# Kernel tuning notes

Hardware: AMD Instinct MI355X
Metric: run time of the kernel (lower is better)

The kernel has to match this reference:

```python
import jax, jax.numpy as jnp
import numpy as np

N_HEADS = 16
D_HEAD = 64


def setup_inputs() -> dict:
    key = jax.random.key(0)
    ks = jax.random.split(key, 9)
    B, L, D = 2, 2048, 1024
    s = 0.02  # small init scale for weights
    return {
        "x": jax.random.normal(ks[0], (B, L, D), jnp.float32),
        "Wq": jax.random.normal(ks[1], (D, D), jnp.float32) * s,
        "bq": jax.random.normal(ks[2], (D,), jnp.float32) * s,
        "Wk": jax.random.normal(ks[3], (D, D), jnp.float32) * s,
        "bk": jax.random.normal(ks[4], (D,), jnp.float32) * s,
        "Wv": jax.random.normal(ks[5], (D, D), jnp.float32) * s,
        "bv": jax.random.normal(ks[6], (D,), jnp.float32) * s,
        "Wo": jax.random.normal(ks[7], (D, D), jnp.float32) * s,
        "bo": jax.random.normal(ks[8], (D,), jnp.float32) * s,
    }


def _alibi_bias(L, n_heads, dtype):
    # slopes m_i = 1 / x**(i+1), x = (2**8)**(1/n_heads)
    x = (2.0 ** 8) ** (1.0 / n_heads)
    slopes = jnp.asarray([1.0 / x ** (i + 1) for i in range(n_heads)], dtype=dtype)
    pos = jnp.arange(L)
    rel = (pos[None, :] - pos[:, None]).astype(dtype)  # [L, L], (j - i)
    return slopes[:, None, None] * rel[None, :, :]      # [H, L, L]


def reference(x, Wq, bq, Wk, bk, Wv, bv, Wo, bo):
    B, L, D = x.shape
    H, dh = N_HEADS, D_HEAD
    scale = dh ** -0.5
    q = (x @ Wq + bq).reshape(B, L, H, dh)
    k = (x @ Wk + bk).reshape(B, L, H, dh)
    v = (x @ Wv + bv).reshape(B, L, H, dh)
    scores = jnp.einsum("blhd,bmhd->bhlm", q, k) * scale  # [B,H,L,L]
    bias = _alibi_bias(L, H, scores.dtype)                 # [H,L,L]
    attn = jax.nn.softmax(scores + bias[None], axis=-1)
    out = jnp.einsum("bhlm,bmhd->blhd", attn, v).reshape(B, L, D)
    return out @ Wo + bo
```

## Files before the change

kernel.cpp:

```cpp
#include <hip/hip_runtime.h>
#include <cstdint>
#include <cstddef>

typedef unsigned short u16;
typedef unsigned int u32;
typedef __bf16 bf16x8 __attribute__((ext_vector_type(8)));
typedef float f32x4 __attribute__((ext_vector_type(4)));
typedef u32 u32x2 __attribute__((ext_vector_type(2)));
typedef u32 u32x4 __attribute__((ext_vector_type(4)));
typedef unsigned short u16x8 __attribute__((ext_vector_type(8)));
typedef short s16x4 __attribute__((ext_vector_type(4)));

__device__ __forceinline__ u16 f2bf(float f) {
    u32 u = __float_as_uint(f);
    u += 0x7fffu + ((u >> 16) & 1u);
    return (u16)(u >> 16);
}

__device__ __forceinline__ float fexp2(float x) {
    float r;
    asm("v_exp_f32 %0, %1" : "=v"(r) : "v"(x));
    return r;
}

__device__ __forceinline__ void gl16(const void* g, void* l) {
    __builtin_amdgcn_global_load_lds(
        (const __attribute__((address_space(1))) unsigned int*)g,
        (__attribute__((address_space(3))) unsigned int*)l, 16, 0, 0);
}

__global__ __launch_bounds__(256) void cvt_all_k(const float* __restrict__ Wq,
                                                 const float* __restrict__ Wk,
                                                 const float* __restrict__ Wv,
                                                 const float* __restrict__ Wo,
                                                 const float* __restrict__ x,
                                                 u16* __restrict__ oqkv,
                                                 u16* __restrict__ oo,
                                                 u16* __restrict__ ox) {
    const int z = blockIdx.z;
    const int bx = blockIdx.x, by = blockIdx.y;
    const int t = threadIdx.x;
    if (z >= 4) {
        int i = ((z - 4) * 256 + by * 16 + bx) * 256 + t;
        const float4* xv = (const float4*)x;
        float4 a = xv[2 * i], b = xv[2 * i + 1];
        ushort4 r0, r1;
        r0.x = f2bf(a.x); r0.y = f2bf(a.y); r0.z = f2bf(a.z); r0.w = f2bf(a.w);
        r1.x = f2bf(b.x); r1.y = f2bf(b.y); r1.z = f2bf(b.z); r1.w = f2bf(b.w);
        ((ushort4*)ox)[2 * i] = r0;
        ((ushort4*)ox)[2 * i + 1] = r1;
        return;
    }
    __shared__ float tile[64][65];
    const float* W = (z == 0) ? Wq : (z == 1) ? Wk : (z == 2) ? Wv : Wo;
    u16* o = (z < 3) ? (oqkv + ((size_t)z << 20)) : oo;
    const int tn = t & 63, tr = t >> 6;
#pragma unroll
    for (int r = 0; r < 16; ++r) {
        int kk = r * 4 + tr;
        tile[kk][tn] = W[(size_t)(by * 64 + kk) * 1024 + bx * 64 + tn];
    }
    __syncthreads();
#pragma unroll
    for (int r = 0; r < 16; ++r) {
        int nn = r * 4 + tr;
        o[(size_t)(bx * 64 + nn) * 1024 + by * 64 + tn] = f2bf(tile[tn][nn]);
    }
}

template <int MODE>
__global__ __launch_bounds__(256) void gemm_k(
    const u16* __restrict__ A, const u16* __restrict__ Bt,
    const float* __restrict__ bias0, const float* __restrict__ bias1,
    const float* __restrict__ bias2,
    u16* __restrict__ oq, u16* __restrict__ ok_, u16* __restrict__ ov,
    float* __restrict__ oc) {
    __shared__ __align__(16) u16 sh[2 * 3 * 128 * 32];
    u16* As = sh;
    u16* Bs = sh + 3 * 128 * 32;
    const int t = threadIdx.x, w = t >> 6, lane = t & 63;
    const int lr = lane & 15, lg = lane >> 4;
    const int brow = blockIdx.x * 128, bcol = blockIdx.y * 128;
    const int wr = w >> 1, wc = w & 1;
    const char* Ab = (const char*)A + (size_t)brow * 2048;
    const char* Bb = (const char*)Bt + (size_t)bcol * 2048;
    const int lrow = lane >> 2;
    const int lcol = (((lane & 3) ^ ((lane >> 3) & 3)) << 4);
    const int r0a = w * 32, r0b = w * 32 + 16;
    const size_t ga = (size_t)(r0a + lrow) * 2048 + lcol;
    const size_t gb = (size_t)(r0b + lrow) * 2048 + lcol;
    const int rsw = ((lg ^ ((lr >> 1) & 3)) << 4);

    f32x4 acc[4][4];
#pragma unroll
    for (int m = 0; m < 4; ++m)
#pragma unroll
        for (int n = 0; n < 4; ++n) acc[m][n] = (f32x4){0.f, 0.f, 0.f, 0.f};

    gl16(Ab + ga, (char*)As + r0a * 64);
    gl16(Ab + gb, (char*)As + r0b * 64);
    gl16(Bb + ga, (char*)Bs + r0a * 64);
    gl16(Bb + gb, (char*)Bs + r0b * 64);
    gl16(Ab + ga + 64, (char*)As + 8192 + r0a * 64);
    gl16(Ab + gb + 64, (char*)As + 8192 + r0b * 64);
    gl16(Bb + ga + 64, (char*)Bs + 8192 + r0a * 64);
    gl16(Bb + gb + 64, (char*)Bs + 8192 + r0b * 64);

    for (int tt = 0; tt < 32; ++tt) {
        if (tt < 31) {
            asm volatile("s_waitcnt vmcnt(4)" ::: "memory");
        } else {
            asm volatile("s_waitcnt vmcnt(0)" ::: "memory");
        }
        __builtin_amdgcn_s_barrier();
        __builtin_amdgcn_sched_barrier(0);
        if (tt < 30) {
            const int nb = (tt + 2) % 3;
            const size_t ko = (size_t)(tt + 2) * 64;
            char* Asn = (char*)As + nb * 8192;
            char* Bsn = (char*)Bs + nb * 8192;
            gl16(Ab + ga + ko, Asn + r0a * 64);
            gl16(Ab + gb + ko, Asn + r0b * 64);
            gl16(Bb + ga + ko, Bsn + r0a * 64);
            gl16(Bb + gb + ko, Bsn + r0b * 64);
        }
        const char* AsB = (const char*)As + (tt % 3) * 8192;
        const char* BsB = (const char*)Bs + (tt % 3) * 8192;
        bf16x8 af[4], bfr[4];
#pragma unroll
        for (int m = 0; m < 4; ++m)
            af[m] = *(const bf16x8*)(AsB + (wr * 64 + m * 16 + lr) * 64 + rsw);
#pragma unroll
        for (int n = 0; n < 4; ++n)
            bfr[n] = *(const bf16x8*)(BsB + (wc * 64 + n * 16 + lr) * 64 + rsw);
#pragma unroll
        for (int m = 0; m < 4; ++m)
#pragma unroll
            for (int n = 0; n < 4; ++n)
                acc[m][n] = __builtin_amdgcn_mfma_f32_16x16x32_bf16(af[m], bfr[n],
                                                                    acc[m][n], 0, 0, 0);
    }

    const float QSCALE = 0.125f * 1.44269504f;
    if (MODE == 0 && bcol >= 2048) {
        const int b = brow >> 11, l0 = brow & 2047;
        __syncthreads();
#pragma unroll
        for (int n = 0; n < 4; ++n) {
            const int cl = wc * 64 + n * 16 + lr;
            const float bb2 = bias2[bcol - 2048 + cl];
#pragma unroll
            for (int m = 0; m < 4; ++m)
#pragma unroll
                for (int r = 0; r < 4; ++r) {
                    int ll = wr * 64 + m * 16 + 4 * lg + r;
                    sh[cl * 136 + ll] = f2bf(acc[m][n][r] + bb2);
                }
        }
        __syncthreads();
        const int rr = t >> 1, hf = t & 1;
        const u16* src = sh + rr * 136 + hf * 64;
        u16* dst = ov + ((size_t)b * 1024 + (bcol - 2048) + rr) * 2048 +
                   l0 + hf * 64;
#pragma unroll
        for (int i = 0; i < 8; ++i)
            *(u16x8*)(dst + i * 8) = *(const u16x8*)(src + i * 8);
        return;
    }
#pragma unroll
    for (int n = 0; n < 4; ++n) {
        const int col = bcol + wc * 64 + n * 16 + lr;
        if (MODE == 0) {
#pragma unroll
            for (int m = 0; m < 4; ++m)
#pragma unroll
                for (int r = 0; r < 4; ++r) {
                    int row = brow + wr * 64 + m * 16 + 4 * lg + r;
                    int b = row >> 11, l = row & 2047;
                    float val = acc[m][n][r];
                    if (col < 1024) {
                        int hh = col >> 6, d = col & 63;
                        oq[(((size_t)b * 16 + hh) * 2048 + l) * 64 + d] =
                            f2bf((val + bias0[col]) * QSCALE);
                    } else {
                        int c = col - 1024, hh = c >> 6, d = c & 63;
                        ok_[(((size_t)b * 16 + hh) * 2048 + l) * 64 + d] =
                            f2bf(val + bias1[c]);
                    }
                }
        } else {
            const float bb = bias0[col];
#pragma unroll
            for (int m = 0; m < 4; ++m)
#pragma unroll
                for (int r = 0; r < 4; ++r) {
                    int row = brow + wr * 64 + m * 16 + 4 * lg + r;
                    oc[(size_t)row * 1024 + col] = acc[m][n][r] + bb;
                }
        }
    }
}

__global__ __launch_bounds__(256, 2) void attn_k(const u16* __restrict__ qg_,
                                                 const u16* __restrict__ kg_,
                                                 const u16* __restrict__ vg_,
                                                 u16* __restrict__ ao) {
    __shared__ __align__(16) u16 smem[32768];
    char* Kbase = (char*)smem;
    char* Vbase = (char*)smem + 32768;
    const int t = threadIdx.x, w = t >> 6, lane = t & 63;
    const int lr = lane & 15, lg = lane >> 4;
    const int bid = blockIdx.y * 16 + blockIdx.x;
    const int qt = (bid >> 3) & 15;
    const int bh = ((bid >> 7) << 3) | (bid & 7);
    const int q0 = qt * 128, h = bh & 15, bb = bh >> 4;
    const float sl2 = exp2f(-0.5f * (float)(h + 1)) * 1.44269504f;

    const char* khead = (const char*)(kg_ + (size_t)bh * 2048 * 64);
    const char* vhead = (const char*)(vg_ + (size_t)bh * 64 * 2048);

    const int krow = lane >> 3, ku = lane & 7;
    const int kso = (w * 32 + krow) * 128 + ((ku ^ (krow & 7)) << 4);
    const int kdo = w * 4096;
    const int vrow = lane >> 4, vgr = lane & 15;
    int vso[4];
#pragma unroll
    for (int i = 0; i < 4; ++i)
        vso[i] = (w * 16 + 4 * i + vrow) * 4096 +
                 ((vgr ^ ((4 * i + vrow) & 7)) << 4);
    const int vdo = w * 4096;

    const char* qpA = (const char*)qg_ +
                      ((size_t)bh * 2048 + q0 + w * 32 + lr) * 128;
    bf16x8 qa0A = *(const bf16x8*)(qpA + lg * 16);
    bf16x8 qa1A = *(const bf16x8*)(qpA + 64 + lg * 16);
    bf16x8 qa0B = *(const bf16x8*)(qpA + 2048 + lg * 16);
    bf16x8 qa1B = *(const bf16x8*)(qpA + 2048 + 64 + lg * 16);

    f32x4 abF2[8];
#pragma unroll
    for (int n = 0; n < 8; ++n)
#pragma unroll
        for (int r = 0; r < 4; ++r)
            abF2[n][r] = sl2 * (float)(n * 16 + 4 * lg + r - 2047) - 16.0f;
    const float ainc = sl2 * 128.0f;
    f32x4 oaccA[4], oaccB[4];
#pragma unroll
    for (int nn = 0; nn < 4; ++nn) {
        oaccA[nn] = (f32x4){0.f, 0.f, 0.f, 0.f};
        oaccB[nn] = (f32x4){0.f, 0.f, 0.f, 0.f};
    }
    f32x4 laccA = (f32x4){0.f, 0.f, 0.f, 0.f};
    f32x4 laccB = (f32x4){0.f, 0.f, 0.f, 0.f};
    const u32x4 ones32 = {0x3F803F80u, 0x3F803F80u, 0x3F803F80u, 0x3F803F80u};
    const bf16x8 onesf = __builtin_bit_cast(bf16x8, ones32);

    {
        char* kd = Kbase + kdo;
        char* vd = Vbase + vdo;
#pragma unroll
        for (int i = 0; i < 4; ++i) gl16(khead + kso + i * 1024, kd + i * 1024);
#pragma unroll
        for (int i = 0; i < 4; ++i) gl16(vhead + vso[i], vd + i * 1024);
    }
    asm volatile("s_waitcnt vmcnt(0)" ::: "memory");
    __builtin_amdgcn_s_barrier();
    __builtin_amdgcn_sched_barrier(0);

    for (int tt = 0; tt < 16; ++tt) {
        if (tt < 15) {
            const char* ks = khead + (size_t)(tt + 1) * 16384;
            const char* vs = vhead + (size_t)(tt + 1) * 256;
            char* kd = Kbase + ((tt + 1) & 1) * 16384 + kdo;
            char* vd = Vbase + ((tt + 1) & 1) * 16384 + vdo;
#pragma unroll
            for (int i = 0; i < 4; ++i) gl16(ks + kso + i * 1024, kd + i * 1024);
#pragma unroll
            for (int i = 0; i < 4; ++i) gl16(vs + vso[i], vd + i * 1024);
        }
        const char* Kc = Kbase + (tt & 1) * 16384;
        const char* Vc = Vbase + (tt & 1) * 16384;

        auto loadVpair = [&](int np, u32x2* dst) {
#pragma unroll
            for (int nn = 0; nn < 4; ++nn) {
                s16x4 v0 = *(const s16x4*)(Vc + (nn * 16 + lr) * 256 +
                                           (((4 * np + (lg >> 1)) ^ (lr & 7)) << 4) +
                                           ((lg & 1) << 3));
                s16x4 v1 = *(const s16x4*)(Vc + (nn * 16 + lr) * 256 +
                                           (((4 * np + 2 + (lg >> 1)) ^ (lr & 7)) << 4) +
                                           ((lg & 1) << 3));
                dst[2 * nn] = __builtin_bit_cast(u32x2, v0);
                dst[2 * nn + 1] = __builtin_bit_cast(u32x2, v1);
            }
        };

        f32x4 saA[8], saB[8];
        __builtin_amdgcn_s_setprio(1);
#pragma unroll
        for (int n = 0; n < 8; ++n) {
            bf16x8 kf = *(const bf16x8*)(Kc + (n * 16 + lr) * 128 +
                                         ((lg ^ (lr & 7)) << 4));
            saA[n] = __builtin_amdgcn_mfma_f32_16x16x32_bf16(kf, qa0A, abF2[n],
                                                             0, 0, 0);
            saB[n] = __builtin_amdgcn_mfma_f32_16x16x32_bf16(kf, qa0B, abF2[n],
                                                             0, 0, 0);
        }
#pragma unroll
        for (int n = 0; n < 8; ++n) {
            bf16x8 kf = *(const bf16x8*)(Kc + (n * 16 + lr) * 128 +
                                         (((4 + lg) ^ (lr & 7)) << 4));
            saA[n] = __builtin_amdgcn_mfma_f32_16x16x32_bf16(kf, qa1A, saA[n],
                                                             0, 0, 0);
            saB[n] = __builtin_amdgcn_mfma_f32_16x16x32_bf16(kf, qa1B, saB[n],
                                                             0, 0, 0);
        }
        __builtin_amdgcn_s_setprio(0);

        u32x2 vP[8], vQ[8];
        loadVpair(0, vP);

#pragma unroll
        for (int n = 0; n < 8; ++n)
#pragma unroll
            for (int r = 0; r < 4; ++r) {
                saA[n][r] = fexp2(saA[n][r]);
                saB[n][r] = fexp2(saB[n][r]);
            }
#pragma unroll
        for (int n = 0; n < 8; ++n) abF2[n] += ainc;

        u32 pA[8][2], pB[8][2];
#pragma unroll
        for (int n = 0; n < 8; ++n) {
            asm("v_cvt_pk_bf16_f32 %0, %1, %2"
                : "=v"(pA[n][0]) : "v"(saA[n][0]), "v"(saA[n][1]));
            asm("v_cvt_pk_bf16_f32 %0, %1, %2"
                : "=v"(pA[n][1]) : "v"(saA[n][2]), "v"(saA[n][3]));
            asm("v_cvt_pk_bf16_f32 %0, %1, %2"
                : "=v"(pB[n][0]) : "v"(saB[n][0]), "v"(saB[n][1]));
            asm("v_cvt_pk_bf16_f32 %0, %1, %2"
                : "=v"(pB[n][1]) : "v"(saB[n][2]), "v"(saB[n][3]));
        }

        auto pvPair = [&](int np, const u32x2* va) {
            const int n0 = 2 * np, n1 = 2 * np + 1;
            u32x4 bwA = {pA[n0][0], pA[n0][1], pA[n1][0], pA[n1][1]};
            u32x4 bwB = {pB[n0][0], pB[n0][1], pB[n1][0], pB[n1][1]};
            bf16x8 pfA = __builtin_bit_cast(bf16x8, bwA);
            bf16x8 pfB = __builtin_bit_cast(bf16x8, bwB);
            laccA = __builtin_amdgcn_mfma_f32_16x16x32_bf16(onesf, pfA,
                                                            laccA, 0, 0, 0);
            laccB = __builtin_amdgcn_mfma_f32_16x16x32_bf16(onesf, pfB,
                                                            laccB, 0, 0, 0);
#pragma unroll
            for (int nn = 0; nn < 4; ++nn) {
                u32x4 aw = {va[2 * nn][0], va[2 * nn][1],
                            va[2 * nn + 1][0], va[2 * nn + 1][1]};
                bf16x8 vaf = __builtin_bit_cast(bf16x8, aw);
                oaccA[nn] = __builtin_amdgcn_mfma_f32_16x16x32_bf16(vaf, pfA,
                                                                    oaccA[nn],
                                                                    0, 0, 0);
                oaccB[nn] = __builtin_amdgcn_mfma_f32_16x16x32_bf16(vaf, pfB,
                                                                    oaccB[nn],
                                                                    0, 0, 0);
            }
        };
        __builtin_amdgcn_s_setprio(1);
        loadVpair(1, vQ);
        pvPair(0, vP);
        loadVpair(2, vP);
        pvPair(1, vQ);
        loadVpair(3, vQ);
        pvPair(2, vP);
        pvPair(3, vQ);
        __builtin_amdgcn_s_setprio(0);

        asm volatile("s_waitcnt vmcnt(0)" ::: "memory");
        __builtin_amdgcn_s_barrier();
        __builtin_amdgcn_sched_barrier(0);
    }

    const float linvA = 1.0f / laccA[0];
    const float linvB = 1.0f / laccB[0];
    u16* ow = smem + w * (32 * 72);
#pragma unroll
    for (int nn = 0; nn < 4; ++nn)
#pragma unroll
        for (int r = 0; r < 4; ++r) {
            ow[lr * 72 + nn * 16 + 4 * lg + r] = f2bf(oaccA[nn][r] * linvA);
            ow[(16 + lr) * 72 + nn * 16 + 4 * lg + r] = f2bf(oaccB[nn][r] * linvB);
        }
    __syncthreads();
    const int q_ = lane >> 2, d0 = (lane & 3) << 4;
    const u16* orowA = smem + w * (32 * 72) + q_ * 72 + d0;
    const u16* orowB = orowA + 16 * 72;
    u16x8 a0 = *(const u16x8*)(orowA);
    u16x8 a1 = *(const u16x8*)(orowA + 8);
    u16x8 b0 = *(const u16x8*)(orowB);
    u16x8 b1 = *(const u16x8*)(orowB + 8);
    size_t gaddr = ((size_t)bb * 2048 + q0 + w * 32 + q_) * 1024 + h * 64 + d0;
    *(u16x8*)(ao + gaddr) = a0;
    *(u16x8*)(ao + gaddr + 8) = a1;
    *(u16x8*)(ao + gaddr + 16 * 1024) = b0;
    *(u16x8*)(ao + gaddr + 16 * 1024 + 8) = b1;
}

extern "C" void kernel_launch(void* const* d_in, const int* in_sizes, int n_in,
                              void* d_out, int out_size, void* d_ws, size_t ws_size,
                              hipStream_t stream) {
    const float* x  = (const float*)d_in[0];
    const float* Wq = (const float*)d_in[1];
    const float* bq = (const float*)d_in[2];
    const float* Wk = (const float*)d_in[3];
    const float* bk = (const float*)d_in[4];
    const float* Wv = (const float*)d_in[5];
    const float* bv = (const float*)d_in[6];
    const float* Wo = (const float*)d_in[7];
    const float* bo = (const float*)d_in[8];

    const size_t MB = 1u << 20;
    if (ws_size < 40 * MB) return;
    char* ws = (char*)d_ws;
    u16* xb    = (u16*)(ws);
    u16* wqkvt = (u16*)(ws + 8 * MB);
    u16* wot   = (u16*)(ws + 14 * MB);
    u16* qb    = (u16*)(ws + 16 * MB);
    u16* kb    = (u16*)(ws + 24 * MB);
    u16* vt    = (u16*)(ws + 32 * MB);
    u16* ao    = xb;

    cvt_all_k<<<dim3(16, 16, 12), 256, 0, stream>>>(Wq, Wk, Wv, Wo, x,
                                                    wqkvt, wot, xb);

    gemm_k<0><<<dim3(32, 24), 256, 0, stream>>>(xb, wqkvt, bq, bk, bv,
                                                qb, kb, vt, nullptr);
    attn_k<<<dim3(16, 32), 256, 0, stream>>>(qb, kb, vt, ao);
    gemm_k<1><<<dim3(32, 8), 256, 0, stream>>>(ao, wot, bo, nullptr, nullptr,
                                               nullptr, nullptr, nullptr,
                                               (float*)d_out);
}
```

Before: 107.5 us.

## Switch GEMM LDS pipeline from triple to double buffering

The projection GEMM now uses two shared-memory stages instead of three. Each iteration prefetches only the next K-tile, then waits for all loads and barriers after the MFMA block. This cuts LDS use, with 17408 elements kept because the epilogue transpose needs that space, which may allow more resident blocks. The cost is less latency hiding, since the loop now waits on vmcnt(0) every iteration instead of leaving one tile in flight.

```diff
diff --git a/kernel.cpp b/kernel.cpp
--- a/kernel.cpp
+++ b/kernel.cpp
@@ -75,9 +75,7 @@
     const float* __restrict__ bias2,
     u16* __restrict__ oq, u16* __restrict__ ok_, u16* __restrict__ ov,
     float* __restrict__ oc) {
-    __shared__ __align__(16) u16 sh[2 * 3 * 128 * 32];
-    u16* As = sh;
-    u16* Bs = sh + 3 * 128 * 32;
+    __shared__ __align__(16) u16 sh[17408];
     const int t = threadIdx.x, w = t >> 6, lane = t & 63;
     const int lr = lane & 15, lg = lane >> 4;
     const int brow = blockIdx.x * 128, bcol = blockIdx.y * 128;
@@ -97,35 +95,25 @@
 #pragma unroll
         for (int n = 0; n < 4; ++n) acc[m][n] = (f32x4){0.f, 0.f, 0.f, 0.f};
 
-    gl16(Ab + ga, (char*)As + r0a * 64);
-    gl16(Ab + gb, (char*)As + r0b * 64);
-    gl16(Bb + ga, (char*)Bs + r0a * 64);
-    gl16(Bb + gb, (char*)Bs + r0b * 64);
-    gl16(Ab + ga + 64, (char*)As + 8192 + r0a * 64);
-    gl16(Ab + gb + 64, (char*)As + 8192 + r0b * 64);
-    gl16(Bb + ga + 64, (char*)Bs + 8192 + r0a * 64);
-    gl16(Bb + gb + 64, (char*)Bs + 8192 + r0b * 64);
+    gl16(Ab + ga, (char*)sh + r0a * 64);
+    gl16(Ab + gb, (char*)sh + r0b * 64);
+    gl16(Bb + ga, (char*)sh + 16384 + r0a * 64);
+    gl16(Bb + gb, (char*)sh + 16384 + r0b * 64);
+    asm volatile("s_waitcnt vmcnt(0)" ::: "memory");
+    __builtin_amdgcn_s_barrier();
+    __builtin_amdgcn_sched_barrier(0);
 
     for (int tt = 0; tt < 32; ++tt) {
         if (tt < 31) {
-            asm volatile("s_waitcnt vmcnt(4)" ::: "memory");
-        } else {
-            asm volatile("s_waitcnt vmcnt(0)" ::: "memory");
-        }
-        __builtin_amdgcn_s_barrier();
-        __builtin_amdgcn_sched_barrier(0);
-        if (tt < 30) {
-            const int nb = (tt + 2) % 3;
-            const size_t ko = (size_t)(tt + 2) * 64;
-            char* Asn = (char*)As + nb * 8192;
-            char* Bsn = (char*)Bs + nb * 8192;
-            gl16(Ab + ga + ko, Asn + r0a * 64);
-            gl16(Ab + gb + ko, Asn + r0b * 64);
-            gl16(Bb + ga + ko, Bsn + r0a * 64);
-            gl16(Bb + gb + ko, Bsn + r0b * 64);
-        }
-        const char* AsB = (const char*)As + (tt % 3) * 8192;
-        const char* BsB = (const char*)Bs + (tt % 3) * 8192;
+            const int nb = (tt + 1) & 1;
+            const size_t ko = (size_t)(tt + 1) * 64;
+            gl16(Ab + ga + ko, (char*)sh + nb * 8192 + r0a * 64);
+            gl16(Ab + gb + ko, (char*)sh + nb * 8192 + r0b * 64);
+            gl16(Bb + ga + ko, (char*)sh + 16384 + nb * 8192 + r0a * 64);
+            gl16(Bb + gb + ko, (char*)sh + 16384 + nb * 8192 + r0b * 64);
+        }
+        const char* AsB = (const char*)sh + (tt & 1) * 8192;
+        const char* BsB = (const char*)sh + 16384 + (tt & 1) * 8192;
         bf16x8 af[4], bfr[4];
 #pragma unroll
         for (int m = 0; m < 4; ++m)
@@ -139,6 +127,9 @@
             for (int n = 0; n < 4; ++n)
                 acc[m][n] = __builtin_amdgcn_mfma_f32_16x16x32_bf16(af[m], bfr[n],
                                                                     acc[m][n], 0, 0, 0);
+        asm volatile("s_waitcnt vmcnt(0)" ::: "memory");
+        __builtin_amdgcn_s_barrier();
+        __builtin_amdgcn_sched_barrier(0);
     }
 
     const float QSCALE = 0.125f * 1.44269504f;
```

Result: slower. 119.4 us (+11.1%).
